# Optimization experiments

Measured on AMD Instinct MI355X. Metric: run time of the kernel, lower is better.

## Reference

```python
import jax, jax.numpy as jnp
import numpy as np

N = 50000      # nodes
E = 800000     # edges (avg degree 16)
F_IN = 512
HID = 128
OUT = 64
NIDX = 1000


def setup_inputs() -> dict:
    key = jax.random.key(0)
    ks = jax.random.split(key, 7)
    x = jax.random.normal(ks[0], (N, F_IN), dtype=jnp.float32)
    edge_src = jax.random.randint(ks[1], (E,), 0, N)
    edge_dst = jax.random.randint(ks[2], (E,), 0, N)
    edge_weight = jax.random.uniform(ks[3], (E,), dtype=jnp.float32)
    W0 = jax.random.normal(ks[4], (F_IN, HID), dtype=jnp.float32) * (1.0 / np.sqrt(F_IN))
    W1 = jax.random.normal(ks[5], (HID, OUT), dtype=jnp.float32) * (1.0 / np.sqrt(HID))
    idx = jax.random.randint(ks[6], (NIDX,), 0, N)
    return {"x": x, "W0": W0, "W1": W1, "edge_weight": edge_weight,
            "edge_src": edge_src, "edge_dst": edge_dst, "idx": idx}


def _spmm(edge_src, edge_dst, edge_weight, h):
    # sparse adj @ h in COO form: gather rows by src, weight, scatter-add to dst
    msg = h[edge_src] * edge_weight[:, None]          # [E, d]
    return jax.ops.segment_sum(msg, edge_dst, num_segments=N)  # [N, d]


def reference(x, W0, W1, edge_weight, edge_src, edge_dst, idx):
    # layer 0: GraphConvolution (x @ W then adj spmm), relu; dropout omitted (eval)
    h = jax.nn.relu(_spmm(edge_src, edge_dst, edge_weight, x @ W0))  # [N, HID]
    # layer 1: final GraphConvolution, no activation
    out = _spmm(edge_src, edge_dst, edge_weight, h @ W1)             # [N, OUT]
    return out[idx]                                                  # [NIDX, OUT]
```

## Files before the change

### kernel.cpp

```cpp
#include <hip/hip_runtime.h>
#include <hip/hip_bf16.h>

#define N_NODES 50000
#define F_IN    512
#define HID     128
#define OUT_F   64
#define NIDX    1000
#define E_NUM   800000
#define CAP     48
#define NGB     782
#define NSCAN2  768

typedef __attribute__((ext_vector_type(8))) short short8;
typedef __attribute__((ext_vector_type(4))) float f32x4;

__device__ inline ushort f2bf(float f) {
    __hip_bfloat16 h = __float2bfloat16(f);
    return *reinterpret_cast<ushort*>(&h);
}
__device__ inline float bf2f(ushort u) {
    return __uint_as_float(((uint)u) << 16);
}
__device__ inline short8 pack8(f32x4 a, f32x4 b) {
    short8 r;
    r[0] = (short)f2bf(a[0]); r[1] = (short)f2bf(a[1]);
    r[2] = (short)f2bf(a[2]); r[3] = (short)f2bf(a[3]);
    r[4] = (short)f2bf(b[0]); r[5] = (short)f2bf(b[1]);
    r[6] = (short)f2bf(b[2]); r[7] = (short)f2bf(b[3]);
    return r;
}

#define GLOAD_LDS16(g, l) __builtin_amdgcn_global_load_lds( \
    (const __attribute__((address_space(1))) unsigned int*)(g), \
    (__attribute__((address_space(3))) unsigned int*)(l), 16, 0, 0)

__global__ __launch_bounds__(256) void prep_kernel(const float* __restrict__ W0,
                                                   ushort* __restrict__ W0t,
                                                   const int* __restrict__ idx,
                                                   ushort* __restrict__ jmap) {
    const int b = blockIdx.x;
    if (b < 64) {
        __shared__ float tl[32][33];
        const int k0 = (b & 15) * 32, n0 = (b >> 4) * 32;
        const int tx = threadIdx.x & 31, ty = threadIdx.x >> 5;
#pragma unroll
        for (int i = 0; i < 4; ++i)
            tl[ty + i * 8][tx] = W0[(size_t)(k0 + ty + i * 8) * HID + n0 + tx];
        __syncthreads();
#pragma unroll
        for (int i = 0; i < 4; ++i) {
            const int n = ty + i * 8;
            W0t[(size_t)(n0 + n) * F_IN + k0 + tx] = f2bf(tl[tx][n]);
        }
    } else {
        const int j = (b - 64) * 256 + threadIdx.x;
        if (j < NIDX) jmap[idx[j]] = (ushort)(j + 1);
    }
}

__global__ __launch_bounds__(256) void bucket_idx_kernel(const int* __restrict__ esrc,
                                                         const int* __restrict__ edst,
                                                         const float* __restrict__ ew,
                                                         const ushort* __restrict__ jmap,
                                                         int* __restrict__ countsA,
                                                         int2* __restrict__ bktA,
                                                         ushort* __restrict__ flags) {
    const int e0 = (blockIdx.x * 256 + threadIdx.x) * 4;
    if (e0 >= E_NUM) return;
    const int4   d4 = *(const int4*)(edst + e0);
    const int4   s4 = *(const int4*)(esrc + e0);
    const float4 w4 = *(const float4*)(ew + e0);
#define DOIT(DD, SS, WW) { const int rep = jmap[DD]; if (rep) { \
        const int r = rep - 1; const int c = atomicAdd(&countsA[r], 1); \
        if (c < CAP) bktA[(size_t)r * CAP + c] = make_int2(SS, __float_as_int(WW)); \
        flags[SS] = 1; } }
    DOIT(d4.x, s4.x, w4.x) DOIT(d4.y, s4.y, w4.y)
    DOIT(d4.z, s4.z, w4.z) DOIT(d4.w, s4.w, w4.w)
#undef DOIT
}

__global__ __launch_bounds__(256, 5) void fused_gemm_scan2(
        const float* __restrict__ x, const ushort* __restrict__ W0t,
        ushort* __restrict__ XW0b,
        const int* __restrict__ esrc, const int* __restrict__ edst,
        const float* __restrict__ ew, const ushort* __restrict__ flags,
        int* __restrict__ countsB, int2* __restrict__ bktB) {
    __shared__ __align__(16) char smem[32768];

    if (blockIdx.x >= NGB) {
        for (int q = (blockIdx.x - NGB) * 256 + threadIdx.x; q < E_NUM / 4;
             q += NSCAN2 * 256) {
            const int e0 = q * 4;
            const int4   d4 = *(const int4*)(edst + e0);
            const int4   s4 = *(const int4*)(esrc + e0);
            const float4 w4 = *(const float4*)(ew + e0);
#define DO2(DD, SS, WW) { if (flags[DD]) { \
        const int c = atomicAdd(&countsB[DD], 1); \
        if (c < CAP) bktB[(size_t)(DD) * CAP + c] = make_int2(SS, __float_as_int(WW)); } }
            DO2(d4.x, s4.x, w4.x) DO2(d4.y, s4.y, w4.y)
            DO2(d4.z, s4.z, w4.z) DO2(d4.w, s4.w, w4.w)
#undef DO2
        }
        return;
    }

    const int t = threadIdx.x;
    const int w = t >> 6, lane = t & 63;
    const int wr = w >> 1, wc = w & 1;
    const int lr = lane & 15, lk = lane >> 4;
    const int m0 = blockIdx.x * 64;

    char* lA = smem;
    char* lB = smem + 16384;
    f32x4 acc[2][4] = {};

    for (int kt = 0; kt < 8; ++kt) {
        const int k0 = kt * 64;
#pragma unroll
        for (int i = 0; i < 4; ++i) {
            const int o = i * 256 + t;
            {
                const int row = o >> 4, c = o & 15;
                int ga = m0 + row; if (ga > N_NODES - 1) ga = N_NODES - 1;
                const float* g = x + (size_t)ga * F_IN + k0 + ((c ^ ((row & 7) << 1)) << 2);
                GLOAD_LDS16(g, lA + (i * 256 + w * 64) * 16);
            }
            {
                const int row = o >> 3, c = o & 7;
                const ushort* g = W0t + (size_t)row * F_IN + k0 + ((c ^ (row & 7)) << 3);
                GLOAD_LDS16(g, lB + (i * 256 + w * 64) * 16);
            }
        }
        __syncthreads();

#pragma unroll
        for (int kk = 0; kk < 2; ++kk) {
            short8 a[2], b[4];
#pragma unroll
            for (int mi = 0; mi < 2; ++mi) {
                const int R = wr * 32 + mi * 16 + lr;
                const int cs = (kk * 8 + lk * 2) ^ ((R & 7) << 1);
                const f32x4 lo = *(const f32x4*)(lA + R * 256 + (cs << 4));
                const f32x4 hi = *(const f32x4*)(lA + R * 256 + (cs << 4) + 16);
                a[mi] = pack8(lo, hi);
            }
#pragma unroll
            for (int ni = 0; ni < 4; ++ni) {
                const int Rb = wc * 64 + ni * 16 + lr;
                const int cs = (kk * 4 + lk) ^ (Rb & 7);
                b[ni] = *(const short8*)(lB + Rb * 128 + (cs << 4));
            }
#pragma unroll
            for (int mi = 0; mi < 2; ++mi)
#pragma unroll
                for (int ni = 0; ni < 4; ++ni)
                    acc[mi][ni] = __builtin_amdgcn_mfma_f32_16x16x32_bf16(
                        a[mi], b[ni], acc[mi][ni], 0, 0, 0);
        }
        __syncthreads();
    }

    float* ep = (float*)smem + w * (16 * 68);
#pragma unroll
    for (int mi = 0; mi < 2; ++mi) {
        __syncthreads();
#pragma unroll
        for (int ni = 0; ni < 4; ++ni)
#pragma unroll
            for (int r = 0; r < 4; ++r)
                ep[(lk * 4 + r) * 68 + ni * 16 + lr] = acc[mi][ni][r];
        __syncthreads();
        const int rr = lane >> 2, cq = lane & 3;
        const int grow = m0 + wr * 32 + mi * 16 + rr;
        alignas(16) float vv[16];
#pragma unroll
        for (int j = 0; j < 4; ++j)
            *(f32x4*)&vv[j * 4] = *(const f32x4*)&ep[rr * 68 + cq * 16 + j * 4];
        if (grow < N_NODES) {
            alignas(16) ushort us[16];
#pragma unroll
            for (int jj = 0; jj < 16; ++jj) us[jj] = f2bf(vv[jj]);
            ushort* orow = XW0b + (size_t)grow * HID + wc * 64 + cq * 16;
            *(uint4*)(orow)     = *(const uint4*)&us[0];
            *(uint4*)(orow + 8) = *(const uint4*)&us[8];
        }
    }
}

__global__ __launch_bounds__(256) void spmm1_kernel(const ushort* __restrict__ XW0b,
                                                    const ushort* __restrict__ flags,
                                                    const int* __restrict__ countsB,
                                                    const int2* __restrict__ bktB,
                                                    ushort* __restrict__ H) {
    const int wv = threadIdx.x >> 6, lane = threadIdx.x & 63;
    const int g = lane >> 4, s = lane & 15;
    for (int n = blockIdx.x * 4 + wv; n < N_NODES; n += gridDim.x * 4) {
        if (!flags[n]) continue;
        const int deg = min(countsB[n], CAP);
        const int2* brow = bktB + (size_t)n * CAP;
        float acc[8] = {};
        for (int c = 0; c < deg; c += 4) {
            const int e = c + g;
            if (e < deg) {
                const int2 p = brow[e];
                const float wt = __int_as_float(p.y);
                const uint4 v = *(const uint4*)(XW0b + (size_t)p.x * HID + s * 8);
                acc[0] += wt * bf2f((ushort)(v.x & 0xffffu));
                acc[1] += wt * bf2f((ushort)(v.x >> 16));
                acc[2] += wt * bf2f((ushort)(v.y & 0xffffu));
                acc[3] += wt * bf2f((ushort)(v.y >> 16));
                acc[4] += wt * bf2f((ushort)(v.z & 0xffffu));
                acc[5] += wt * bf2f((ushort)(v.z >> 16));
                acc[6] += wt * bf2f((ushort)(v.w & 0xffffu));
                acc[7] += wt * bf2f((ushort)(v.w >> 16));
            }
        }
#pragma unroll
        for (int j = 0; j < 8; ++j) {
            acc[j] += __shfl_xor(acc[j], 16);
            acc[j] += __shfl_xor(acc[j], 32);
        }
        if (g == 0) {
            uint4 o;
            o.x = (uint)f2bf(fmaxf(acc[0], 0.f)) | ((uint)f2bf(fmaxf(acc[1], 0.f)) << 16);
            o.y = (uint)f2bf(fmaxf(acc[2], 0.f)) | ((uint)f2bf(fmaxf(acc[3], 0.f)) << 16);
            o.z = (uint)f2bf(fmaxf(acc[4], 0.f)) | ((uint)f2bf(fmaxf(acc[5], 0.f)) << 16);
            o.w = (uint)f2bf(fmaxf(acc[6], 0.f)) | ((uint)f2bf(fmaxf(acc[7], 0.f)) << 16);
            *(uint4*)(H + (size_t)n * HID + s * 8) = o;
        }
    }
}

__global__ __launch_bounds__(64) void spmm2_kernel(const ushort* __restrict__ H,
                                                   const float* __restrict__ W1,
                                                   const int* __restrict__ idx,
                                                   const ushort* __restrict__ jmap,
                                                   const int* __restrict__ countsA,
                                                   const int2* __restrict__ bktA,
                                                   float* __restrict__ outp) {
    __shared__ float aggs[HID];
    const int j = blockIdx.x, lane = threadIdx.x;
    const int r = (int)jmap[idx[j]] - 1;
    const int deg = min(countsA[r], CAP);
    float a0 = 0.f, a1 = 0.f;
    for (int c = 0; c < deg; ++c) {
        const int2 p = bktA[(size_t)r * CAP + c];
        const float wt = __int_as_float(p.y);
        const uint v = *(const uint*)(H + (size_t)p.x * HID + 2 * lane);
        a0 += wt * bf2f((ushort)(v & 0xffffu));
        a1 += wt * bf2f((ushort)(v >> 16));
    }
    aggs[2 * lane] = a0; aggs[2 * lane + 1] = a1;
    __syncthreads();
    float s = 0.f;
#pragma unroll 8
    for (int k = 0; k < HID; ++k) s += aggs[k] * W1[k * OUT_F + lane];
    outp[(size_t)j * OUT_F + lane] = s;
}

extern "C" void kernel_launch(void* const* d_in, const int* in_sizes, int n_in,
                              void* d_out, int out_size, void* d_ws, size_t ws_size,
                              hipStream_t stream) {
    const float* x    = (const float*)d_in[0];
    const float* W0   = (const float*)d_in[1];
    const float* W1   = (const float*)d_in[2];
    const float* ew   = (const float*)d_in[3];
    const int*   esrc = (const int*)d_in[4];
    const int*   edst = (const int*)d_in[5];
    const int*   idx  = (const int*)d_in[6];
    float* outp = (float*)d_out;

    char* ws = (char*)d_ws;
    ushort* XW0b   = (ushort*)(ws);
    ushort* H      = (ushort*)(ws + 12800000);
    ushort* W0t    = (ushort*)(ws + 25600000);
    int2*   bktA   = (int2*)  (ws + 25731072);
    int2*   bktB   = (int2*)  (ws + 26115072);
    char*   zbase  = ws + 45315072;
    int*    countsA = (int*)   (zbase);
    int*    countsB = (int*)   (zbase + 4096);
    ushort* flags   = (ushort*)(zbase + 208896);
    ushort* jmap    = (ushort*)(zbase + 309248);
    hipMemsetAsync(zbase, 0, 409600, stream);

    prep_kernel      <<<68, 256, 0, stream>>>(W0, W0t, idx, jmap);
    bucket_idx_kernel<<<(E_NUM / 4 + 255) / 256, 256, 0, stream>>>(esrc, edst, ew, jmap, countsA, bktA, flags);
    fused_gemm_scan2 <<<NGB + NSCAN2, 256, 0, stream>>>(
                         x, W0t, XW0b, esrc, edst, ew, flags, countsB, bktB);
    spmm1_kernel     <<<2048, 256, 0, stream>>>(XW0b, flags, countsB, bktB, H);
    spmm2_kernel     <<<NIDX, 64, 0, stream>>>(H, W1, idx, jmap, countsA, bktA, outp);
}
```

Measured before the change: 84.52 us.

## Double-buffer A tile via register prefetch in fused GEMM K-loop

Replaces direct global-to-LDS loads of the x tile with register prefetch two steps ahead and a double-buffered LDS A region, so global loads overlap MFMA work. B remains single-buffered via direct LDS loads, and waits use explicit vmcnt/lgkmcnt and raw barriers. LDS grows to 48KB and launch bounds drop from 5 to 3 blocks per CU, which reduces occupancy for both the GEMM and the edge-scan blocks in the same kernel.

```diff
diff --git a/kernel.cpp b/kernel.cpp
--- a/kernel.cpp
+++ b/kernel.cpp
@@ -79,13 +79,13 @@
 #undef DOIT
 }
 
-__global__ __launch_bounds__(256, 5) void fused_gemm_scan2(
+__global__ __launch_bounds__(256, 3) void fused_gemm_scan2(
         const float* __restrict__ x, const ushort* __restrict__ W0t,
         ushort* __restrict__ XW0b,
         const int* __restrict__ esrc, const int* __restrict__ edst,
         const float* __restrict__ ew, const ushort* __restrict__ flags,
         int* __restrict__ countsB, int2* __restrict__ bktB) {
-    __shared__ __align__(16) char smem[32768];
+    __shared__ __align__(16) char smem[49152];
 
     if (blockIdx.x >= NGB) {
         for (int q = (blockIdx.x - NGB) * 256 + threadIdx.x; q < E_NUM / 4;
@@ -110,29 +110,50 @@
     const int lr = lane & 15, lk = lane >> 4;
     const int m0 = blockIdx.x * 64;
 
-    char* lA = smem;
-    char* lB = smem + 16384;
+    char* lA  = smem;
+    char* lBl = smem + 32768;
     f32x4 acc[2][4] = {};
-
-    for (int kt = 0; kt < 8; ++kt) {
-        const int k0 = kt * 64;
+    float4 fa[4];
+
+    auto loadA = [&](int kt) {
 #pragma unroll
         for (int i = 0; i < 4; ++i) {
             const int o = i * 256 + t;
-            {
-                const int row = o >> 4, c = o & 15;
-                int ga = m0 + row; if (ga > N_NODES - 1) ga = N_NODES - 1;
-                const float* g = x + (size_t)ga * F_IN + k0 + ((c ^ ((row & 7) << 1)) << 2);
-                GLOAD_LDS16(g, lA + (i * 256 + w * 64) * 16);
-            }
-            {
-                const int row = o >> 3, c = o & 7;
-                const ushort* g = W0t + (size_t)row * F_IN + k0 + ((c ^ (row & 7)) << 3);
-                GLOAD_LDS16(g, lB + (i * 256 + w * 64) * 16);
-            }
-        }
-        __syncthreads();
-
+            const int row = o >> 4, c = o & 15;
+            int ga = m0 + row; if (ga > N_NODES - 1) ga = N_NODES - 1;
+            fa[i] = *(const float4*)(x + (size_t)ga * F_IN + kt * 64 + c * 4);
+        }
+    };
+    auto writeA = [&](int buf) {
+#pragma unroll
+        for (int i = 0; i < 4; ++i) {
+            const int o = i * 256 + t;
+            const int row = o >> 4, c = o & 15;
+            *(float4*)(lA + buf * 16384 + row * 256 + ((c ^ ((row & 7) << 1)) << 4)) = fa[i];
+        }
+    };
+    auto stageB = [&](int kt) {
+#pragma unroll
+        for (int i = 0; i < 4; ++i) {
+            const int o = i * 256 + t;
+            const int row = o >> 3, c = o & 7;
+            const ushort* g = W0t + (size_t)row * F_IN + kt * 64 + ((c ^ (row & 7)) << 3);
+            GLOAD_LDS16(g, lBl + (i * 256 + w * 64) * 16);
+        }
+    };
+
+    loadA(0);
+    writeA(0);
+    stageB(0);
+    loadA(1);
+    asm volatile("s_waitcnt vmcnt(4)" ::: "memory");
+    asm volatile("s_waitcnt lgkmcnt(0)" ::: "memory");
+    __builtin_amdgcn_s_barrier();
+
+#pragma unroll
+    for (int kt = 0; kt < 8; ++kt) {
+        const int cur = kt & 1;
+        const char* Ab = lA + cur * 16384;
 #pragma unroll
         for (int kk = 0; kk < 2; ++kk) {
             short8 a[2], b[4];
@@ -140,15 +161,15 @@
             for (int mi = 0; mi < 2; ++mi) {
                 const int R = wr * 32 + mi * 16 + lr;
                 const int cs = (kk * 8 + lk * 2) ^ ((R & 7) << 1);
-                const f32x4 lo = *(const f32x4*)(lA + R * 256 + (cs << 4));
-                const f32x4 hi = *(const f32x4*)(lA + R * 256 + (cs << 4) + 16);
+                const f32x4 lo = *(const f32x4*)(Ab + R * 256 + (cs << 4));
+                const f32x4 hi = *(const f32x4*)(Ab + R * 256 + (cs << 4) + 16);
                 a[mi] = pack8(lo, hi);
             }
 #pragma unroll
             for (int ni = 0; ni < 4; ++ni) {
                 const int Rb = wc * 64 + ni * 16 + lr;
                 const int cs = (kk * 4 + lk) ^ (Rb & 7);
-                b[ni] = *(const short8*)(lB + Rb * 128 + (cs << 4));
+                b[ni] = *(const short8*)(lBl + Rb * 128 + (cs << 4));
             }
 #pragma unroll
             for (int mi = 0; mi < 2; ++mi)
@@ -157,8 +178,21 @@
                     acc[mi][ni] = __builtin_amdgcn_mfma_f32_16x16x32_bf16(
                         a[mi], b[ni], acc[mi][ni], 0, 0, 0);
         }
-        __syncthreads();
-    }
+        if (kt < 7) {
+            __builtin_amdgcn_s_barrier();
+            writeA(cur ^ 1);
+            stageB(kt + 1);
+            if (kt + 2 <= 7) {
+                loadA(kt + 2);
+                asm volatile("s_waitcnt vmcnt(4)" ::: "memory");
+            } else {
+                asm volatile("s_waitcnt vmcnt(0)" ::: "memory");
+            }
+            asm volatile("s_waitcnt lgkmcnt(0)" ::: "memory");
+            __builtin_amdgcn_s_barrier();
+        }
+    }
+    __syncthreads();
 
     float* ep = (float*)smem + w * (16 * 68);
 #pragma unroll
```

Result: slower. 104.9 us (+24.1%).

## Overlap first edge scan with GEMM and run second scan standalone

Applied to the files above, without the earlier changes.

Moves the edge-bucketing scan for the output-index destinations (scan1) into the GEMM launch as extra blocks, and pulls the flagged-destination scan (scan2) out into its own kernel that runs after the GEMM. Scan1 now hides behind the dense GEMM instead of running serially before it. Scan2 previously overlapped the GEMM and now runs serially, so the net effect depends on which scan is cheaper to expose.

```diff
diff --git a/kernel.cpp b/kernel.cpp
--- a/kernel.cpp
+++ b/kernel.cpp
@@ -8,6 +8,7 @@
 #define NIDX    1000
 #define E_NUM   800000
 #define CAP     48
+#define NSC1    256
 #define NGB     782
 #define NSCAN2  768
 
@@ -58,48 +59,28 @@
     }
 }
 
-__global__ __launch_bounds__(256) void bucket_idx_kernel(const int* __restrict__ esrc,
-                                                         const int* __restrict__ edst,
-                                                         const float* __restrict__ ew,
-                                                         const ushort* __restrict__ jmap,
-                                                         int* __restrict__ countsA,
-                                                         int2* __restrict__ bktA,
-                                                         ushort* __restrict__ flags) {
-    const int e0 = (blockIdx.x * 256 + threadIdx.x) * 4;
-    if (e0 >= E_NUM) return;
-    const int4   d4 = *(const int4*)(edst + e0);
-    const int4   s4 = *(const int4*)(esrc + e0);
-    const float4 w4 = *(const float4*)(ew + e0);
+__global__ __launch_bounds__(256, 5) void fused_gemm_scan1(
+        const float* __restrict__ x, const ushort* __restrict__ W0t,
+        ushort* __restrict__ XW0b,
+        const int* __restrict__ esrc, const int* __restrict__ edst,
+        const float* __restrict__ ew, const ushort* __restrict__ jmap,
+        int* __restrict__ countsA, int2* __restrict__ bktA,
+        ushort* __restrict__ flags) {
+    __shared__ __align__(16) char smem[32768];
+
+    if (blockIdx.x < NSC1) {
+        for (int q = blockIdx.x * 256 + threadIdx.x; q < E_NUM / 4; q += NSC1 * 256) {
+            const int e0 = q * 4;
+            const int4   d4 = *(const int4*)(edst + e0);
+            const int4   s4 = *(const int4*)(esrc + e0);
+            const float4 w4 = *(const float4*)(ew + e0);
 #define DOIT(DD, SS, WW) { const int rep = jmap[DD]; if (rep) { \
         const int r = rep - 1; const int c = atomicAdd(&countsA[r], 1); \
         if (c < CAP) bktA[(size_t)r * CAP + c] = make_int2(SS, __float_as_int(WW)); \
         flags[SS] = 1; } }
-    DOIT(d4.x, s4.x, w4.x) DOIT(d4.y, s4.y, w4.y)
-    DOIT(d4.z, s4.z, w4.z) DOIT(d4.w, s4.w, w4.w)
+            DOIT(d4.x, s4.x, w4.x) DOIT(d4.y, s4.y, w4.y)
+            DOIT(d4.z, s4.z, w4.z) DOIT(d4.w, s4.w, w4.w)
 #undef DOIT
-}
-
-__global__ __launch_bounds__(256, 5) void fused_gemm_scan2(
-        const float* __restrict__ x, const ushort* __restrict__ W0t,
-        ushort* __restrict__ XW0b,
-        const int* __restrict__ esrc, const int* __restrict__ edst,
-        const float* __restrict__ ew, const ushort* __restrict__ flags,
-        int* __restrict__ countsB, int2* __restrict__ bktB) {
-    __shared__ __align__(16) char smem[32768];
-
-    if (blockIdx.x >= NGB) {
-        for (int q = (blockIdx.x - NGB) * 256 + threadIdx.x; q < E_NUM / 4;
-             q += NSCAN2 * 256) {
-            const int e0 = q * 4;
-            const int4   d4 = *(const int4*)(edst + e0);
-            const int4   s4 = *(const int4*)(esrc + e0);
-            const float4 w4 = *(const float4*)(ew + e0);
-#define DO2(DD, SS, WW) { if (flags[DD]) { \
-        const int c = atomicAdd(&countsB[DD], 1); \
-        if (c < CAP) bktB[(size_t)(DD) * CAP + c] = make_int2(SS, __float_as_int(WW)); } }
-            DO2(d4.x, s4.x, w4.x) DO2(d4.y, s4.y, w4.y)
-            DO2(d4.z, s4.z, w4.z) DO2(d4.w, s4.w, w4.w)
-#undef DO2
         }
         return;
     }
@@ -108,7 +89,7 @@
     const int w = t >> 6, lane = t & 63;
     const int wr = w >> 1, wc = w & 1;
     const int lr = lane & 15, lk = lane >> 4;
-    const int m0 = blockIdx.x * 64;
+    const int m0 = (blockIdx.x - NSC1) * 64;
 
     char* lA = smem;
     char* lB = smem + 16384;
@@ -184,6 +165,26 @@
             *(uint4*)(orow)     = *(const uint4*)&us[0];
             *(uint4*)(orow + 8) = *(const uint4*)&us[8];
         }
+    }
+}
+
+__global__ __launch_bounds__(256) void scan2_kernel(const int* __restrict__ esrc,
+                                                    const int* __restrict__ edst,
+                                                    const float* __restrict__ ew,
+                                                    const ushort* __restrict__ flags,
+                                                    int* __restrict__ countsB,
+                                                    int2* __restrict__ bktB) {
+    for (int q = blockIdx.x * 256 + threadIdx.x; q < E_NUM / 4; q += NSCAN2 * 256) {
+        const int e0 = q * 4;
+        const int4   d4 = *(const int4*)(edst + e0);
+        const int4   s4 = *(const int4*)(esrc + e0);
+        const float4 w4 = *(const float4*)(ew + e0);
+#define DO2(DD, SS, WW) { if (flags[DD]) { \
+        const int c = atomicAdd(&countsB[DD], 1); \
+        if (c < CAP) bktB[(size_t)(DD) * CAP + c] = make_int2(SS, __float_as_int(WW)); } }
+        DO2(d4.x, s4.x, w4.x) DO2(d4.y, s4.y, w4.y)
+        DO2(d4.z, s4.z, w4.z) DO2(d4.w, s4.w, w4.w)
+#undef DO2
     }
 }
 
@@ -283,10 +284,10 @@
     ushort* jmap    = (ushort*)(zbase + 309248);
     hipMemsetAsync(zbase, 0, 409600, stream);
 
-    prep_kernel      <<<68, 256, 0, stream>>>(W0, W0t, idx, jmap);
-    bucket_idx_kernel<<<(E_NUM / 4 + 255) / 256, 256, 0, stream>>>(esrc, edst, ew, jmap, countsA, bktA, flags);
-    fused_gemm_scan2 <<<NGB + NSCAN2, 256, 0, stream>>>(
-                         x, W0t, XW0b, esrc, edst, ew, flags, countsB, bktB);
-    spmm1_kernel     <<<2048, 256, 0, stream>>>(XW0b, flags, countsB, bktB, H);
-    spmm2_kernel     <<<NIDX, 64, 0, stream>>>(H, W1, idx, jmap, countsA, bktA, outp);
-}
+    prep_kernel     <<<68, 256, 0, stream>>>(W0, W0t, idx, jmap);
+    fused_gemm_scan1<<<NSC1 + NGB, 256, 0, stream>>>(
+                        x, W0t, XW0b, esrc, edst, ew, jmap, countsA, bktA, flags);
+    scan2_kernel    <<<NSCAN2, 256, 0, stream>>>(esrc, edst, ew, flags, countsB, bktB);
+    spmm1_kernel    <<<2048, 256, 0, stream>>>(XW0b, flags, countsB, bktB, H);
+    spmm2_kernel    <<<NIDX, 64, 0, stream>>>(H, W1, idx, jmap, countsA, bktA, outp);
+}
```

New measurement: 88.80 us. +5.1%, slower.

## Stage full-K x tile in LDS with 32-row blocks in fused GEMM

Applied to the files above, without the earlier changes.

The x@W0 GEMM now uses 32-row tiles instead of 64. It preloads each tile's full 512-wide row strip of x into a 64KB LDS buffer in one batch of async loads, and only W0t is streamed per 32-wide k-step. This doubles the number of GEMM blocks and aims to cut per-k-step load/sync overhead on the large x read. In exchange, LDS use rises to 72KB, occupancy drops to 2 blocks per CU, and W0t is re-read by twice as many blocks.

```diff
diff --git a/kernel.cpp b/kernel.cpp
--- a/kernel.cpp
+++ b/kernel.cpp
@@ -8,7 +8,7 @@
 #define NIDX    1000
 #define E_NUM   800000
 #define CAP     48
-#define NGB     782
+#define NGB     1563
 #define NSCAN2  768
 
 typedef __attribute__((ext_vector_type(8))) short short8;
@@ -79,13 +79,13 @@
 #undef DOIT
 }
 
-__global__ __launch_bounds__(256, 5) void fused_gemm_scan2(
+__global__ __launch_bounds__(256, 2) void fused_gemm_scan2(
         const float* __restrict__ x, const ushort* __restrict__ W0t,
         ushort* __restrict__ XW0b,
         const int* __restrict__ esrc, const int* __restrict__ edst,
         const float* __restrict__ ew, const ushort* __restrict__ flags,
         int* __restrict__ countsB, int2* __restrict__ bktB) {
-    __shared__ __align__(16) char smem[32768];
+    __shared__ __align__(16) char smem[73728];
 
     if (blockIdx.x >= NGB) {
         for (int q = (blockIdx.x - NGB) * 256 + threadIdx.x; q < E_NUM / 4;
@@ -108,82 +108,70 @@
     const int w = t >> 6, lane = t & 63;
     const int wr = w >> 1, wc = w & 1;
     const int lr = lane & 15, lk = lane >> 4;
-    const int m0 = blockIdx.x * 64;
+    const int m0 = blockIdx.x * 32;
 
     char* lA = smem;
-    char* lB = smem + 16384;
-    f32x4 acc[2][4] = {};
-
-    for (int kt = 0; kt < 8; ++kt) {
-        const int k0 = kt * 64;
-#pragma unroll
-        for (int i = 0; i < 4; ++i) {
+    char* lB = smem + 65536;
+    f32x4 acc[4] = {};
+
+#pragma unroll
+    for (int i = 0; i < 16; ++i) {
+        const int o = i * 256 + t;
+        const int row = o >> 7, c = o & 127;
+        int ga = m0 + row; if (ga > N_NODES - 1) ga = N_NODES - 1;
+        const float* g = x + (size_t)ga * F_IN + ((c ^ ((row & 7) << 1)) << 2);
+        GLOAD_LDS16(g, lA + (i * 256 + w * 64) * 16);
+    }
+
+    for (int kt = 0; kt < 16; ++kt) {
+#pragma unroll
+        for (int i = 0; i < 2; ++i) {
             const int o = i * 256 + t;
-            {
-                const int row = o >> 4, c = o & 15;
-                int ga = m0 + row; if (ga > N_NODES - 1) ga = N_NODES - 1;
-                const float* g = x + (size_t)ga * F_IN + k0 + ((c ^ ((row & 7) << 1)) << 2);
-                GLOAD_LDS16(g, lA + (i * 256 + w * 64) * 16);
-            }
-            {
-                const int row = o >> 3, c = o & 7;
-                const ushort* g = W0t + (size_t)row * F_IN + k0 + ((c ^ (row & 7)) << 3);
-                GLOAD_LDS16(g, lB + (i * 256 + w * 64) * 16);
-            }
+            const int row = o >> 2, c = o & 3;
+            const ushort* g = W0t + (size_t)row * F_IN + kt * 32 + ((c ^ (row & 3)) << 3);
+            GLOAD_LDS16(g, lB + (i * 256 + w * 64) * 16);
         }
         __syncthreads();
 
-#pragma unroll
-        for (int kk = 0; kk < 2; ++kk) {
-            short8 a[2], b[4];
-#pragma unroll
-            for (int mi = 0; mi < 2; ++mi) {
-                const int R = wr * 32 + mi * 16 + lr;
-                const int cs = (kk * 8 + lk * 2) ^ ((R & 7) << 1);
-                const f32x4 lo = *(const f32x4*)(lA + R * 256 + (cs << 4));
-                const f32x4 hi = *(const f32x4*)(lA + R * 256 + (cs << 4) + 16);
-                a[mi] = pack8(lo, hi);
-            }
-#pragma unroll
-            for (int ni = 0; ni < 4; ++ni) {
-                const int Rb = wc * 64 + ni * 16 + lr;
-                const int cs = (kk * 4 + lk) ^ (Rb & 7);
-                b[ni] = *(const short8*)(lB + Rb * 128 + (cs << 4));
-            }
-#pragma unroll
-            for (int mi = 0; mi < 2; ++mi)
-#pragma unroll
-                for (int ni = 0; ni < 4; ++ni)
-                    acc[mi][ni] = __builtin_amdgcn_mfma_f32_16x16x32_bf16(
-                        a[mi], b[ni], acc[mi][ni], 0, 0, 0);
-        }
+        short8 b[4];
+        const int R = wr * 16 + lr;
+        const int L = kt * 8 + lk * 2;
+        const int sw = (R & 7) << 1;
+        const f32x4 lo = *(const f32x4*)(lA + R * 2048 + ((L ^ sw) << 4));
+        const f32x4 hi = *(const f32x4*)(lA + R * 2048 + (((L + 1) ^ sw) << 4));
+        const short8 a = pack8(lo, hi);
+#pragma unroll
+        for (int ni = 0; ni < 4; ++ni) {
+            const int Rb = wc * 64 + ni * 16 + lr;
+            b[ni] = *(const short8*)(lB + Rb * 64 + ((lk ^ (Rb & 3)) << 4));
+        }
+#pragma unroll
+        for (int ni = 0; ni < 4; ++ni)
+            acc[ni] = __builtin_amdgcn_mfma_f32_16x16x32_bf16(a, b[ni], acc[ni], 0, 0, 0);
         __syncthreads();
     }
 
     float* ep = (float*)smem + w * (16 * 68);
-#pragma unroll
-    for (int mi = 0; mi < 2; ++mi) {
-        __syncthreads();
-#pragma unroll
-        for (int ni = 0; ni < 4; ++ni)
-#pragma unroll
-            for (int r = 0; r < 4; ++r)
-                ep[(lk * 4 + r) * 68 + ni * 16 + lr] = acc[mi][ni][r];
-        __syncthreads();
-        const int rr = lane >> 2, cq = lane & 3;
-        const int grow = m0 + wr * 32 + mi * 16 + rr;
-        alignas(16) float vv[16];
-#pragma unroll
-        for (int j = 0; j < 4; ++j)
-            *(f32x4*)&vv[j * 4] = *(const f32x4*)&ep[rr * 68 + cq * 16 + j * 4];
-        if (grow < N_NODES) {
-            alignas(16) ushort us[16];
-#pragma unroll
-            for (int jj = 0; jj < 16; ++jj) us[jj] = f2bf(vv[jj]);
-            ushort* orow = XW0b + (size_t)grow * HID + wc * 64 + cq * 16;
-            *(uint4*)(orow)     = *(const uint4*)&us[0];
-            *(uint4*)(orow + 8) = *(const uint4*)&us[8];
-        }
+    __syncthreads();
+#pragma unroll
+    for (int ni = 0; ni < 4; ++ni)
+#pragma unroll
+        for (int r = 0; r < 4; ++r)
+            ep[(lk * 4 + r) * 68 + ni * 16 + lr] = acc[ni][r];
+    __syncthreads();
+    const int rr = lane >> 2, cq = lane & 3;
+    const int grow = m0 + wr * 16 + rr;
+    alignas(16) float vv[16];
+#pragma unroll
+    for (int j = 0; j < 4; ++j)
+        *(f32x4*)&vv[j * 4] = *(const f32x4*)&ep[rr * 68 + cq * 16 + j * 4];
+    if (grow < N_NODES) {
+        alignas(16) ushort us[16];
+#pragma unroll
+        for (int jj = 0; jj < 16; ++jj) us[jj] = f2bf(vv[jj]);
+        ushort* orow = XW0b + (size_t)grow * HID + wc * 64 + cq * 16;
+        *(uint4*)(orow)     = *(const uint4*)&us[0];
+        *(uint4*)(orow + 8) = *(const uint4*)&us[8];
     }
 }
 
```

After: 105.0 us. +24.2%, slower.
